# Optimization experiments

Measured on AMD Instinct MI355X. Metric: run time of the kernel, lower is better.

The kernel has to match this reference:

```python
import jax, jax.numpy as jnp
import numpy as np

N_NODES = 50000
N_EDGES = 600000
HIDDEN = 128
NUM_FEAT = 3
NUM_CLASSES = 2
NUM_GRAPHS = 512


def setup_inputs() -> dict:
    key = jax.random.key(0)
    ks = jax.random.split(key, 12)
    x = jax.random.normal(ks[0], (N_NODES, NUM_FEAT), dtype=jnp.float32)
    edge_index = jax.random.randint(ks[1], (2, N_EDGES), 0, N_NODES, dtype=jnp.int64)
    batch = jnp.sort(jax.random.randint(ks[2], (N_NODES,), 0, NUM_GRAPHS, dtype=jnp.int64))

    def glorot(k, fan_in, fan_out):
        s = jnp.sqrt(6.0 / (fan_in + fan_out)).astype(jnp.float32)
        return jax.random.uniform(k, (fan_in, fan_out), jnp.float32, -s, s)

    return {
        "x": x,
        "W1": glorot(ks[3], NUM_FEAT, HIDDEN), "b1": jnp.zeros((HIDDEN,), jnp.float32),
        "W2": glorot(ks[4], HIDDEN, HIDDEN),  "b2": jnp.zeros((HIDDEN,), jnp.float32),
        "W3": glorot(ks[5], HIDDEN, HIDDEN),  "b3": jnp.zeros((HIDDEN,), jnp.float32),
        "W4": glorot(ks[6], HIDDEN, HIDDEN),  "b4": jnp.zeros((HIDDEN,), jnp.float32),
        "linW": glorot(ks[7], HIDDEN, NUM_CLASSES), "linb": jnp.zeros((NUM_CLASSES,), jnp.float32),
        "edge_index": edge_index,
        "batch": batch,
        "num_graphs": NUM_GRAPHS,
    }


def gcn_conv(x, W, b, src, dst, n_nodes):
    # PyG GCNConv: h = x W; out = D^-1/2 (A + I) D^-1/2 h + b
    h = x @ W                                    # [N, out]
    deg = jnp.zeros((n_nodes,), h.dtype).at[dst].add(1.0) + 1.0  # with self-loops
    dinv = jax.lax.rsqrt(deg)                    # [N]
    norm = dinv[src] * dinv[dst]                 # [E]
    msg = h[src] * norm[:, None]                 # gather + scale
    agg = jax.ops.segment_sum(msg, dst, num_segments=n_nodes)  # scatter-add
    agg = agg + h * (dinv * dinv)[:, None]       # self-loop contribution
    return agg + b


def reference(x, W1, b1, W2, b2, W3, b3, W4, b4, linW, linb, edge_index, batch, num_graphs):
    src, dst = edge_index[0], edge_index[1]
    n = x.shape[0]
    h = jax.nn.relu(gcn_conv(x, W1, b1, src, dst, n))
    h = jax.nn.relu(gcn_conv(h, W2, b2, src, dst, n))
    h = jax.nn.relu(gcn_conv(h, W3, b3, src, dst, n))
    h = gcn_conv(h, W4, b4, src, dst, n)
    # global_mean_pool over graphs
    sums = jax.ops.segment_sum(h, batch, num_segments=num_graphs)
    cnts = jax.ops.segment_sum(jnp.ones((n,), h.dtype), batch, num_segments=num_graphs)
    pooled = sums / jnp.maximum(cnts, 1.0)[:, None]
    # dropout is identity in eval mode
    return pooled @ linW + linb
```

## Files before the change

kernel.cpp:

```cpp
#include <hip/hip_runtime.h>
#include <hip/hip_bf16.h>

#define HID 128
#define NGRAPH 512

typedef __attribute__((ext_vector_type(8))) short short8;
typedef __attribute__((ext_vector_type(4))) float f32x4;

__device__ inline unsigned int f2bf(float f) {
    unsigned int u = __float_as_uint(f);
    return (u + 0x7FFFu + ((u >> 16) & 1u)) >> 16;
}
__device__ inline float bflo(unsigned int w) { return __uint_as_float(w << 16); }
__device__ inline float bfhi(unsigned int w) { return __uint_as_float(w & 0xFFFF0000u); }


__global__ void k_zero(int* __restrict__ p, int n) {
    int i = blockIdx.x * blockDim.x + threadIdx.x;
    if (i < n) p[i] = 0;
}

__global__ void k_count(const int* __restrict__ ei, int* __restrict__ deg,
                        int* __restrict__ epos, int E) {
    int e = blockIdx.x * blockDim.x + threadIdx.x;
    if (e < E) epos[e] = atomicAdd(&deg[ei[E + e]], 1);
}

__device__ inline void wcast_body(const float* __restrict__ W,
                                  unsigned short* __restrict__ Wt) {
    int t = threadIdx.x;
#pragma unroll
    for (int i = 0; i < 16; ++i) {
        int flat = i * 1024 + t;
        int n = flat >> 7, k = flat & 127;
        Wt[n * HID + k] = (unsigned short)f2bf(W[k * HID + n]);
    }
}

__global__ void k_bsum(const int* __restrict__ deg, int* __restrict__ bsum, int n,
                       int nblocks, const float* __restrict__ W4,
                       const float* __restrict__ linW, const float* __restrict__ b4,
                       const float* __restrict__ linb, float* __restrict__ W4p,
                       float* __restrict__ b4p, const float* __restrict__ W2,
                       const float* __restrict__ W3, unsigned short* __restrict__ Wt2,
                       unsigned short* __restrict__ Wt3) {
    if ((int)blockIdx.x == nblocks) {
        int idx = threadIdx.x;
        if (idx < 256) {
            int k = idx >> 1, c = idx & 1;
            float a = 0.0f;
            for (int j = 0; j < HID; ++j) a = fmaf(W4[k * HID + j], linW[j * 2 + c], a);
            W4p[idx] = a;
            if (idx < 2) {
                float b = 0.0f;
                for (int j = 0; j < HID; ++j) b = fmaf(b4[j], linW[j * 2 + idx], b);
                b4p[idx] = b + linb[idx];
            }
        }
        return;
    }
    if ((int)blockIdx.x == nblocks + 1) { wcast_body(W2, Wt2); return; }
    if ((int)blockIdx.x == nblocks + 2) { wcast_body(W3, Wt3); return; }
    int i = blockIdx.x * 1024 + threadIdx.x;
    int v = (i < n) ? deg[i] : 0;
#pragma unroll
    for (int off = 32; off; off >>= 1) v += __shfl_down(v, off);
    __shared__ int ws[16];
    int wid = threadIdx.x >> 6, lane = threadIdx.x & 63;
    if (lane == 0) ws[wid] = v;
    __syncthreads();
    if (threadIdx.x == 0) {
        int s = 0;
#pragma unroll
        for (int w = 0; w < 16; ++w) s += ws[w];
        bsum[blockIdx.x] = s;
    }
}

__global__ void k_scan2(const int* __restrict__ deg, const int* __restrict__ bsum,
                        int* __restrict__ row_start, float* __restrict__ dinv,
                        const float* __restrict__ x, float* __restrict__ Xs,
                        int n, int nblocks) {
    __shared__ int s_off, s_tot;
    __shared__ int ws[16];
    if (threadIdx.x < 64) {
        int v = ((int)threadIdx.x < blockIdx.x) ? bsum[threadIdx.x] : 0;
#pragma unroll
        for (int off = 32; off; off >>= 1) v += __shfl_down(v, off);
        if (threadIdx.x == 0) s_off = v;
    } else if (threadIdx.x < 128 && blockIdx.x == 0) {
        int l = threadIdx.x - 64;
        int v = (l < nblocks) ? bsum[l] : 0;
#pragma unroll
        for (int off = 32; off; off >>= 1) v += __shfl_down(v, off);
        if (l == 0) s_tot = v;
    }
    int i = blockIdx.x * 1024 + threadIdx.x;
    int v = (i < n) ? deg[i] : 0;
    if (i < n) {
        float dv = rsqrtf((float)v + 1.0f);
        dinv[i] = dv;
        float4 r;
        r.x = x[i * 3 + 0] * dv;
        r.y = x[i * 3 + 1] * dv;
        r.z = x[i * 3 + 2] * dv;
        r.w = 0.0f;
        *(float4*)&Xs[i * 4] = r;
    }
    int xx = v;
    int lane = threadIdx.x & 63, wid = threadIdx.x >> 6;
#pragma unroll
    for (int off = 1; off < 64; off <<= 1) {
        int t = __shfl_up(xx, off);
        if (lane >= off) xx += t;
    }
    if (lane == 63) ws[wid] = xx;
    __syncthreads();
    int wo = 0;
    for (int w = 0; w < wid; ++w) wo += ws[w];
    int excl = s_off + wo + xx - v;
    if (i < n) row_start[i] = excl;
    if (blockIdx.x == 0 && threadIdx.x == 0) row_start[n] = s_tot;
}

__global__ void k_fill(const int* __restrict__ ei, const int* __restrict__ row_start,
                       const int* __restrict__ epos, int* __restrict__ src_sorted, int E) {
    int e = blockIdx.x * blockDim.x + threadIdx.x;
    if (e < E) {
        int s = ei[e];
        int d = ei[E + e];
        src_sorted[row_start[d] + epos[e]] = s;
    }
}


__global__ __launch_bounds__(256) void k_gather3w(const float* __restrict__ Xs,
                                                  const int* __restrict__ row_start,
                                                  const int* __restrict__ src_sorted,
                                                  const float* __restrict__ dinv,
                                                  float* __restrict__ xa, int n) {
    int t = blockIdx.x * blockDim.x + threadIdx.x;
    int v = t >> 3, sub = t & 7;
    if (v >= n) return;
    float a0 = 0.f, a1 = 0.f, a2 = 0.f;
    int e0 = row_start[v], e1 = row_start[v + 1];
    for (int e = e0 + sub; e < e1; e += 8) {
        int s = src_sorted[e];
        float4 xs = *(const float4*)&Xs[s * 4];
        a0 += xs.x; a1 += xs.y; a2 += xs.z;
    }
#pragma unroll
    for (int off = 4; off; off >>= 1) {
        a0 += __shfl_down(a0, off);
        a1 += __shfl_down(a1, off);
        a2 += __shfl_down(a2, off);
    }
    if (sub == 0) {
        float dv = dinv[v];
        float4 xv = *(const float4*)&Xs[v * 4];
        xa[v * 4 + 0] = (a0 + xv.x) * dv;
        xa[v * 4 + 1] = (a1 + xv.y) * dv;
        xa[v * 4 + 2] = (a2 + xv.z) * dv;
    }
}

__global__ void k_feat(const float* __restrict__ xa, const float* __restrict__ W1,
                       const float* __restrict__ b1, unsigned int* __restrict__ Act16,
                       int n) {
    int idx = blockIdx.x * blockDim.x + threadIdx.x;
    int v = idx >> 6, cp = idx & 63;
    unsigned int w = 0;
    if (v < n) {
        float x0 = xa[v * 4 + 0], x1 = xa[v * 4 + 1], x2 = xa[v * 4 + 2];
        int c0 = cp * 2, c1 = c0 + 1;
        float r0 = fmaf(x0, W1[c0], fmaf(x1, W1[HID + c0], fmaf(x2, W1[2 * HID + c0], b1[c0])));
        float r1 = fmaf(x0, W1[c1], fmaf(x1, W1[HID + c1], fmaf(x2, W1[2 * HID + c1], b1[c1])));
        w = f2bf(fmaxf(r0, 0.f)) | (f2bf(fmaxf(r1, 0.f)) << 16);
    }
    Act16[idx] = w;
}

__global__ __launch_bounds__(256) void k_gemm_mfma(const unsigned short* __restrict__ X,
                                                   const unsigned short* __restrict__ Wtg,
                                                   const float* __restrict__ dinv,
                                                   unsigned short* __restrict__ Hout) {
    __shared__ unsigned short Wt[HID * HID];
    {
        int nrow = threadIdx.x >> 1, s = threadIdx.x & 1;
        int xr = (nrow & 7) << 3;
#pragma unroll
        for (int i = 0; i < 8; ++i) {
            int b16 = s * 64 + i * 8;
            uint4 src = *(const uint4*)&Wtg[nrow * HID + b16];
            *(uint4*)&Wt[nrow * HID + (b16 ^ xr)] = src;
        }
    }
    __syncthreads();

    int w    = threadIdx.x >> 6;
    int lane = threadIdx.x & 63;
    int g    = lane >> 4;
    int mr   = lane & 15;
    size_t row0 = (size_t)blockIdx.x * 64;
    size_t arow = row0 + w * 16 + mr;

    short8 a[4];
#pragma unroll
    for (int ks = 0; ks < 4; ++ks)
        a[ks] = *(const short8*)&X[arow * HID + ks * 32 + g * 8];

    f32x4 acc[8];
#pragma unroll
    for (int nt = 0; nt < 8; ++nt) acc[nt] = (f32x4){0.f, 0.f, 0.f, 0.f};

#pragma unroll
    for (int nt = 0; nt < 8; ++nt) {
        int nrow = nt * 16 + mr;
        int xr = (nrow & 7) << 3;
        short8 b[4];
#pragma unroll
        for (int ks = 0; ks < 4; ++ks)
            b[ks] = *(const short8*)&Wt[nrow * HID + ((ks * 32 + g * 8) ^ xr)];
#pragma unroll
        for (int ks = 0; ks < 4; ++ks)
            acc[nt] = __builtin_amdgcn_mfma_f32_16x16x32_bf16(a[ks], b[ks], acc[nt], 0, 0, 0);
    }

    __syncthreads();
    {
        int rrb = w * 16 + g * 4;
#pragma unroll
        for (int j = 0; j < 4; ++j) {
            int rr = rrb + j;
            float dv = dinv[row0 + rr];
#pragma unroll
            for (int nt = 0; nt < 8; ++nt) {
                int col = nt * 16 + mr;
                int idx = rr * HID + ((col & 7) | ((((col >> 3)) ^ (rr & 7)) << 3));
                Wt[idx] = (unsigned short)f2bf(acc[nt][j] * dv);
            }
        }
    }
    __syncthreads();
    {
        int rr = threadIdx.x >> 2, s = threadIdx.x & 3;
        int xr = (rr & 7) << 3;
#pragma unroll
        for (int i = 0; i < 4; ++i) {
            int b16 = s * 32 + i * 8;
            uint4 v = *(const uint4*)&Wt[rr * HID + (b16 ^ xr)];
            *(uint4*)&Hout[(row0 + rr) * HID + b16] = v;
        }
    }
}

__global__ __launch_bounds__(256) void k_gather(const unsigned short* __restrict__ Hs,
                                                const int* __restrict__ row_start,
                                                const int* __restrict__ src_sorted,
                                                const float* __restrict__ dinv,
                                                const float* __restrict__ bias,
                                                unsigned short* __restrict__ Aout, int n) {
    int wid  = (blockIdx.x * blockDim.x + threadIdx.x) >> 6;
    int lane = threadIdx.x & 63;
    int half = lane >> 5, hl = lane & 31;
    int v0 = wid * 2;
    if (v0 >= n) return;
    int v  = v0 + half;
    bool real = (v < n);
    int vc = real ? v : v0;
    int e0 = row_start[vc];
    int e1 = row_start[vc + 1];
    int deg = e1 - e0;
    int myidx = (hl < deg) ? src_sorted[e0 + hl] : vc;
    float4 acc = make_float4(0.f, 0.f, 0.f, 0.f);
    int dcap = (deg < 32) ? deg : 32;
    for (int base = 0; base < dcap; base += 16) {
        uint2 h[16];
        float m[16];
#pragma unroll
        for (int j = 0; j < 16; ++j) {
            int ej = base + j;
            int sj = __shfl(myidx, (half << 5) | ej);
            m[j] = (ej < deg) ? 1.0f : 0.0f;
            h[j] = *(const uint2*)&Hs[(size_t)sj * HID + hl * 4];
        }
#pragma unroll
        for (int j = 0; j < 16; ++j) {
            acc.x = fmaf(bflo(h[j].x), m[j], acc.x);
            acc.y = fmaf(bfhi(h[j].x), m[j], acc.y);
            acc.z = fmaf(bflo(h[j].y), m[j], acc.z);
            acc.w = fmaf(bfhi(h[j].y), m[j], acc.w);
        }
    }
    for (int e = e0 + 32; e < e1; ++e) {
        int sj = src_sorted[e];
        uint2 h = *(const uint2*)&Hs[(size_t)sj * HID + hl * 4];
        acc.x += bflo(h.x); acc.y += bfhi(h.x);
        acc.z += bflo(h.y); acc.w += bfhi(h.y);
    }
    float dv = dinv[vc];
    uint2 sv = *(const uint2*)&Hs[(size_t)vc * HID + hl * 4];
    float4 bb = *(const float4*)&bias[hl * 4];
    float ox = fmaxf(fmaf(acc.x + bflo(sv.x), dv, bb.x), 0.0f);
    float oy = fmaxf(fmaf(acc.y + bfhi(sv.x), dv, bb.y), 0.0f);
    float oz = fmaxf(fmaf(acc.z + bflo(sv.y), dv, bb.z), 0.0f);
    float ow = fmaxf(fmaf(acc.w + bfhi(sv.y), dv, bb.w), 0.0f);
    if (real) {
        uint2 o2;
        o2.x = f2bf(ox) | (f2bf(oy) << 16);
        o2.y = f2bf(oz) | (f2bf(ow) << 16);
        *(uint2*)&Aout[(size_t)v * HID + hl * 4] = o2;
    }
}

__global__ __launch_bounds__(256) void k_gather_proj(const unsigned short* __restrict__ Hs,
                                                     const int* __restrict__ row_start,
                                                     const int* __restrict__ src_sorted,
                                                     const float* __restrict__ dinv,
                                                     const float* __restrict__ bias,
                                                     const float* __restrict__ W4p,
                                                     float* __restrict__ P3s, int n) {
    int wid  = (blockIdx.x * blockDim.x + threadIdx.x) >> 6;
    int lane = threadIdx.x & 63;
    int half = lane >> 5, hl = lane & 31;
    int v0 = wid * 2;
    if (v0 >= n) return;
    int v  = v0 + half;
    bool real = (v < n);
    int vc = real ? v : v0;
    int e0 = row_start[vc];
    int e1 = row_start[vc + 1];
    int deg = e1 - e0;
    int myidx = (hl < deg) ? src_sorted[e0 + hl] : vc;
    float4 acc = make_float4(0.f, 0.f, 0.f, 0.f);
    int dcap = (deg < 32) ? deg : 32;
    for (int base = 0; base < dcap; base += 16) {
        uint2 h[16];
        float m[16];
#pragma unroll
        for (int j = 0; j < 16; ++j) {
            int ej = base + j;
            int sj = __shfl(myidx, (half << 5) | ej);
            m[j] = (ej < deg) ? 1.0f : 0.0f;
            h[j] = *(const uint2*)&Hs[(size_t)sj * HID + hl * 4];
        }
#pragma unroll
        for (int j = 0; j < 16; ++j) {
            acc.x = fmaf(bflo(h[j].x), m[j], acc.x);
            acc.y = fmaf(bfhi(h[j].x), m[j], acc.y);
            acc.z = fmaf(bflo(h[j].y), m[j], acc.z);
            acc.w = fmaf(bfhi(h[j].y), m[j], acc.w);
        }
    }
    for (int e = e0 + 32; e < e1; ++e) {
        int sj = src_sorted[e];
        uint2 h = *(const uint2*)&Hs[(size_t)sj * HID + hl * 4];
        acc.x += bflo(h.x); acc.y += bfhi(h.x);
        acc.z += bflo(h.y); acc.w += bfhi(h.y);
    }
    float dv = dinv[vc];
    uint2 sv = *(const uint2*)&Hs[(size_t)vc * HID + hl * 4];
    float4 bb = *(const float4*)&bias[hl * 4];
    float ox = fmaxf(fmaf(acc.x + bflo(sv.x), dv, bb.x), 0.0f);
    float oy = fmaxf(fmaf(acc.y + bfhi(sv.x), dv, bb.y), 0.0f);
    float oz = fmaxf(fmaf(acc.z + bflo(sv.y), dv, bb.z), 0.0f);
    float ow = fmaxf(fmaf(acc.w + bfhi(sv.y), dv, bb.w), 0.0f);
    float4 wA = *(const float4*)&W4p[hl * 8 + 0];
    float4 wB = *(const float4*)&W4p[hl * 8 + 4];
    float p0 = ox * wA.x + oy * wA.z + oz * wB.x + ow * wB.z;
    float p1 = ox * wA.y + oy * wA.w + oz * wB.y + ow * wB.w;
#pragma unroll
    for (int off = 16; off; off >>= 1) {
        p0 += __shfl_down(p0, off);
        p1 += __shfl_down(p1, off);
    }
    if (hl == 0 && real) *(float2*)&P3s[v * 2] = make_float2(p0 * dv, p1 * dv);
}

__global__ __launch_bounds__(256) void k_gather2(const float* __restrict__ P3s,
                                                 const int* __restrict__ row_start,
                                                 const int* __restrict__ src_sorted,
                                                 const float* __restrict__ dinv,
                                                 float* __restrict__ A2, int n) {
    int t = blockIdx.x * blockDim.x + threadIdx.x;
    int v = t >> 3, sub = t & 7;
    if (v >= n) return;
    float ax = 0.f, ay = 0.f;
    int e0 = row_start[v], e1 = row_start[v + 1];
    for (int e = e0 + sub; e < e1; e += 8) {
        int s = src_sorted[e];
        float2 ps = *(const float2*)&P3s[s * 2];
        ax += ps.x;
        ay += ps.y;
    }
#pragma unroll
    for (int off = 4; off; off >>= 1) {
        ax += __shfl_down(ax, off);
        ay += __shfl_down(ay, off);
    }
    if (sub == 0) {
        float dv = dinv[v];
        float2 pv = *(const float2*)&P3s[v * 2];
        *(float2*)&A2[v * 2] = make_float2((ax + pv.x) * dv, (ay + pv.y) * dv);
    }
}

__global__ void k_poolg(const float* __restrict__ A2, const int* __restrict__ batch,
                        const float* __restrict__ b4p, float* __restrict__ out, int n) {
    int g = blockIdx.x;
    int lane = threadIdx.x;
    int lo = 0, hi = n;
    while (lo < hi) { int m = (lo + hi) >> 1; if (batch[m] < g) lo = m + 1; else hi = m; }
    int start = lo;
    hi = n;
    while (lo < hi) { int m = (lo + hi) >> 1; if (batch[m] < g + 1) lo = m + 1; else hi = m; }
    int end = lo;
    float sx = 0.f, sy = 0.f;
    for (int i = start + lane; i < end; i += 64) {
        float2 a = *(const float2*)&A2[i * 2];
        sx += a.x;
        sy += a.y;
    }
#pragma unroll
    for (int off = 32; off; off >>= 1) {
        sx += __shfl_down(sx, off);
        sy += __shfl_down(sy, off);
    }
    if (lane == 0) {
        float inv = 1.0f / fmaxf((float)(end - start), 1.0f);
        out[g * 2 + 0] = sx * inv + b4p[0];
        out[g * 2 + 1] = sy * inv + b4p[1];
    }
}


extern "C" void kernel_launch(void* const* d_in, const int* in_sizes, int n_in,
                              void* d_out, int out_size, void* d_ws, size_t ws_size,
                              hipStream_t stream) {
    const float* x    = (const float*)d_in[0];
    const float* W1   = (const float*)d_in[1];
    const float* b1   = (const float*)d_in[2];
    const float* W2   = (const float*)d_in[3];
    const float* b2   = (const float*)d_in[4];
    const float* W3   = (const float*)d_in[5];
    const float* b3   = (const float*)d_in[6];
    const float* W4   = (const float*)d_in[7];
    const float* b4   = (const float*)d_in[8];
    const float* linW = (const float*)d_in[9];
    const float* linb = (const float*)d_in[10];
    const int*   ei   = (const int*)d_in[11];
    const int*   batch= (const int*)d_in[12];
    float* out        = (float*)d_out;

    const int N = in_sizes[0] / 3;
    const int E = in_sizes[11] / 2;
    const int NPAD = ((N + 127) / 128) * 128;
    const int NB1024 = (N + 1023) / 1024;

    float* ws = (float*)d_ws;
    float* dinv       = ws;
    int*   deg_i      = (int*)(ws + 50176);
    int*   row_start  = (int*)(ws + 100352);
    int*   epos       = (int*)(ws + 150784);
    int*   bsum       = (int*)(ws + 750848);
    float* W4p        = ws + 750912;
    float* b4p        = ws + 751168;
    int*   src_sorted = (int*)(ws + 751232);
    float* Xa         = ws + 1351296;
    float* A2         = Xa;
    float* P3s        = ws + 1552000;
    unsigned short* Hbuf16 = (unsigned short*)(ws + 1652352);
    float* Xs         = ws + 1652352;
    unsigned short* Act16 = (unsigned short*)(ws + 1652352 + (size_t)NPAD * 64);
    unsigned short* Wt2g  = (unsigned short*)(ws + 1652352 + 2 * (size_t)NPAD * 64);
    unsigned short* Wt3g  = Wt2g + HID * HID;

    const int B = 256;

    k_zero<<<(N + B - 1) / B, B, 0, stream>>>(deg_i, N);
    k_count<<<(E + B - 1) / B, B, 0, stream>>>(ei, deg_i, epos, E);
    k_bsum<<<NB1024 + 3, 1024, 0, stream>>>(deg_i, bsum, N, NB1024, W4, linW, b4, linb,
                                            W4p, b4p, W2, W3, Wt2g, Wt3g);
    k_scan2<<<NB1024, 1024, 0, stream>>>(deg_i, bsum, row_start, dinv, x, Xs, N, NB1024);
    k_fill<<<(E + B - 1) / B, B, 0, stream>>>(ei, row_start, epos, src_sorted, E);

    const int gatherBlocks = (N + 7) / 8;
    const int g8Blocks     = (N * 8 + B - 1) / B;
    const int gemmBlocks   = NPAD / 64;

    k_gather3w<<<g8Blocks, B, 0, stream>>>(Xs, row_start, src_sorted, dinv, Xa, N);
    k_feat<<<(NPAD * 64) / B, B, 0, stream>>>(Xa, W1, b1, (unsigned int*)Act16, N);
    k_gemm_mfma<<<gemmBlocks, B, 0, stream>>>(Act16, Wt2g, dinv, Hbuf16);
    k_gather<<<gatherBlocks, B, 0, stream>>>(Hbuf16, row_start, src_sorted, dinv, b2, Act16, N);
    k_gemm_mfma<<<gemmBlocks, B, 0, stream>>>(Act16, Wt3g, dinv, Hbuf16);
    k_gather_proj<<<gatherBlocks, B, 0, stream>>>(Hbuf16, row_start, src_sorted, dinv, b3, W4p, P3s, N);
    k_gather2<<<g8Blocks, B, 0, stream>>>(P3s, row_start, src_sorted, dinv, A2, N);
    k_poolg<<<NGRAPH, 64, 0, stream>>>(A2, batch, b4p, out, N);
}
```

Measured before the change: 169.4 us.

## Fuse setup, layer-1 and tail kernels to cut launch count

Measured after the change: 169.8 us. About the same (+0.3%).

```diff
diff --git a/kernel.cpp b/kernel.cpp
--- a/kernel.cpp
+++ b/kernel.cpp
@@ -14,17 +14,6 @@
 __device__ inline float bflo(unsigned int w) { return __uint_as_float(w << 16); }
 __device__ inline float bfhi(unsigned int w) { return __uint_as_float(w & 0xFFFF0000u); }
 
-
-__global__ void k_zero(int* __restrict__ p, int n) {
-    int i = blockIdx.x * blockDim.x + threadIdx.x;
-    if (i < n) p[i] = 0;
-}
-
-__global__ void k_count(const int* __restrict__ ei, int* __restrict__ deg,
-                        int* __restrict__ epos, int E) {
-    int e = blockIdx.x * blockDim.x + threadIdx.x;
-    if (e < E) epos[e] = atomicAdd(&deg[ei[E + e]], 1);
-}
 
 __device__ inline void wcast_body(const float* __restrict__ W,
                                   unsigned short* __restrict__ Wt) {
@@ -37,14 +26,13 @@
     }
 }
 
-__global__ void k_bsum(const int* __restrict__ deg, int* __restrict__ bsum, int n,
-                       int nblocks, const float* __restrict__ W4,
-                       const float* __restrict__ linW, const float* __restrict__ b4,
-                       const float* __restrict__ linb, float* __restrict__ W4p,
-                       float* __restrict__ b4p, const float* __restrict__ W2,
-                       const float* __restrict__ W3, unsigned short* __restrict__ Wt2,
-                       unsigned short* __restrict__ Wt3) {
-    if ((int)blockIdx.x == nblocks) {
+__global__ void k_setup1(int* __restrict__ deg, int n, int nzb,
+                         const float* __restrict__ W4, const float* __restrict__ linW,
+                         const float* __restrict__ b4, const float* __restrict__ linb,
+                         float* __restrict__ W4p, float* __restrict__ b4p,
+                         const float* __restrict__ W2, const float* __restrict__ W3,
+                         unsigned short* __restrict__ Wt2, unsigned short* __restrict__ Wt3) {
+    if ((int)blockIdx.x == nzb) {
         int idx = threadIdx.x;
         if (idx < 256) {
             int k = idx >> 1, c = idx & 1;
@@ -59,41 +47,40 @@
         }
         return;
     }
-    if ((int)blockIdx.x == nblocks + 1) { wcast_body(W2, Wt2); return; }
-    if ((int)blockIdx.x == nblocks + 2) { wcast_body(W3, Wt3); return; }
+    if ((int)blockIdx.x == nzb + 1) { wcast_body(W2, Wt2); return; }
+    if ((int)blockIdx.x == nzb + 2) { wcast_body(W3, Wt3); return; }
     int i = blockIdx.x * 1024 + threadIdx.x;
-    int v = (i < n) ? deg[i] : 0;
-#pragma unroll
-    for (int off = 32; off; off >>= 1) v += __shfl_down(v, off);
+    if (i < n) deg[i] = 0;
+}
+
+__global__ void k_count(const int* __restrict__ ei, int* __restrict__ deg,
+                        int* __restrict__ epos, int E) {
+    int e = blockIdx.x * blockDim.x + threadIdx.x;
+    if (e < E) epos[e] = atomicAdd(&deg[ei[E + e]], 1);
+}
+
+__global__ void k_scan2b(const int* __restrict__ deg, int* __restrict__ row_start,
+                         float* __restrict__ dinv, const float* __restrict__ x,
+                         float* __restrict__ Xs, int n, int nblocks) {
+    __shared__ int rs[16];
     __shared__ int ws[16];
-    int wid = threadIdx.x >> 6, lane = threadIdx.x & 63;
-    if (lane == 0) ws[wid] = v;
-    __syncthreads();
-    if (threadIdx.x == 0) {
-        int s = 0;
-#pragma unroll
-        for (int w = 0; w < 16; ++w) s += ws[w];
-        bsum[blockIdx.x] = s;
-    }
-}
-
-__global__ void k_scan2(const int* __restrict__ deg, const int* __restrict__ bsum,
-                        int* __restrict__ row_start, float* __restrict__ dinv,
-                        const float* __restrict__ x, float* __restrict__ Xs,
-                        int n, int nblocks) {
-    __shared__ int s_off, s_tot;
-    __shared__ int ws[16];
-    if (threadIdx.x < 64) {
-        int v = ((int)threadIdx.x < blockIdx.x) ? bsum[threadIdx.x] : 0;
-#pragma unroll
-        for (int off = 32; off; off >>= 1) v += __shfl_down(v, off);
-        if (threadIdx.x == 0) s_off = v;
-    } else if (threadIdx.x < 128 && blockIdx.x == 0) {
-        int l = threadIdx.x - 64;
-        int v = (l < nblocks) ? bsum[l] : 0;
-#pragma unroll
-        for (int off = 32; off; off >>= 1) v += __shfl_down(v, off);
-        if (l == 0) s_tot = v;
+    __shared__ int s_off_sh;
+    int lane = threadIdx.x & 63, wid = threadIdx.x >> 6;
+    {
+        int before = blockIdx.x * 1024;
+        int p = 0;
+        for (int i = threadIdx.x; i < before; i += 1024) p += deg[i];
+#pragma unroll
+        for (int off = 32; off; off >>= 1) p += __shfl_down(p, off);
+        if (lane == 0) rs[wid] = p;
+        __syncthreads();
+        if (threadIdx.x == 0) {
+            int s = 0;
+#pragma unroll
+            for (int w = 0; w < 16; ++w) s += rs[w];
+            s_off_sh = s;
+        }
+        __syncthreads();
     }
     int i = blockIdx.x * 1024 + threadIdx.x;
     int v = (i < n) ? deg[i] : 0;
@@ -108,7 +95,6 @@
         *(float4*)&Xs[i * 4] = r;
     }
     int xx = v;
-    int lane = threadIdx.x & 63, wid = threadIdx.x >> 6;
 #pragma unroll
     for (int off = 1; off < 64; off <<= 1) {
         int t = __shfl_up(xx, off);
@@ -118,9 +104,14 @@
     __syncthreads();
     int wo = 0;
     for (int w = 0; w < wid; ++w) wo += ws[w];
-    int excl = s_off + wo + xx - v;
+    int excl = s_off_sh + wo + xx - v;
     if (i < n) row_start[i] = excl;
-    if (blockIdx.x == 0 && threadIdx.x == 0) row_start[n] = s_tot;
+    if ((int)blockIdx.x == nblocks - 1 && threadIdx.x == 0) {
+        int ct = 0;
+#pragma unroll
+        for (int w = 0; w < 16; ++w) ct += ws[w];
+        row_start[n] = s_off_sh + ct;
+    }
 }
 
 __global__ void k_fill(const int* __restrict__ ei, const int* __restrict__ row_start,
@@ -133,21 +124,25 @@
     }
 }
 
-
-__global__ __launch_bounds__(256) void k_gather3w(const float* __restrict__ Xs,
-                                                  const int* __restrict__ row_start,
-                                                  const int* __restrict__ src_sorted,
-                                                  const float* __restrict__ dinv,
-                                                  float* __restrict__ xa, int n) {
-    int t = blockIdx.x * blockDim.x + threadIdx.x;
-    int v = t >> 3, sub = t & 7;
-    if (v >= n) return;
+__global__ __launch_bounds__(256) void k_l1(const float* __restrict__ Xs,
+                                            const int* __restrict__ row_start,
+                                            const int* __restrict__ src_sorted,
+                                            const float* __restrict__ dinv,
+                                            const float* __restrict__ W1,
+                                            const float* __restrict__ b1,
+                                            unsigned int* __restrict__ Act16, int n) {
+    __shared__ float xs[32][4];
+    int v0 = blockIdx.x * 32;
+    int vl0 = threadIdx.x >> 3, sub = threadIdx.x & 7;
+    int v = v0 + vl0;
     float a0 = 0.f, a1 = 0.f, a2 = 0.f;
-    int e0 = row_start[v], e1 = row_start[v + 1];
-    for (int e = e0 + sub; e < e1; e += 8) {
-        int s = src_sorted[e];
-        float4 xs = *(const float4*)&Xs[s * 4];
-        a0 += xs.x; a1 += xs.y; a2 += xs.z;
+    if (v < n) {
+        int e0 = row_start[v], e1 = row_start[v + 1];
+        for (int e = e0 + sub; e < e1; e += 8) {
+            int s = src_sorted[e];
+            float4 xv = *(const float4*)&Xs[s * 4];
+            a0 += xv.x; a1 += xv.y; a2 += xv.z;
+        }
     }
 #pragma unroll
     for (int off = 4; off; off >>= 1) {
@@ -155,29 +150,29 @@
         a1 += __shfl_down(a1, off);
         a2 += __shfl_down(a2, off);
     }
-    if (sub == 0) {
+    if (sub == 0 && v < n) {
         float dv = dinv[v];
         float4 xv = *(const float4*)&Xs[v * 4];
-        xa[v * 4 + 0] = (a0 + xv.x) * dv;
-        xa[v * 4 + 1] = (a1 + xv.y) * dv;
-        xa[v * 4 + 2] = (a2 + xv.z) * dv;
-    }
-}
-
-__global__ void k_feat(const float* __restrict__ xa, const float* __restrict__ W1,
-                       const float* __restrict__ b1, unsigned int* __restrict__ Act16,
-                       int n) {
-    int idx = blockIdx.x * blockDim.x + threadIdx.x;
-    int v = idx >> 6, cp = idx & 63;
-    unsigned int w = 0;
-    if (v < n) {
-        float x0 = xa[v * 4 + 0], x1 = xa[v * 4 + 1], x2 = xa[v * 4 + 2];
-        int c0 = cp * 2, c1 = c0 + 1;
-        float r0 = fmaf(x0, W1[c0], fmaf(x1, W1[HID + c0], fmaf(x2, W1[2 * HID + c0], b1[c0])));
-        float r1 = fmaf(x0, W1[c1], fmaf(x1, W1[HID + c1], fmaf(x2, W1[2 * HID + c1], b1[c1])));
-        w = f2bf(fmaxf(r0, 0.f)) | (f2bf(fmaxf(r1, 0.f)) << 16);
-    }
-    Act16[idx] = w;
+        xs[vl0][0] = (a0 + xv.x) * dv;
+        xs[vl0][1] = (a1 + xv.y) * dv;
+        xs[vl0][2] = (a2 + xv.z) * dv;
+    }
+    __syncthreads();
+    unsigned int base = (unsigned int)v0 * 64;
+#pragma unroll
+    for (int i = 0; i < 8; ++i) {
+        int flat = i * 256 + threadIdx.x;
+        int vl = flat >> 6, cp = flat & 63;
+        unsigned int w = 0;
+        if (v0 + vl < n) {
+            float x0 = xs[vl][0], x1 = xs[vl][1], x2 = xs[vl][2];
+            int c0 = cp * 2, c1 = c0 + 1;
+            float r0 = fmaf(x0, W1[c0], fmaf(x1, W1[HID + c0], fmaf(x2, W1[2 * HID + c0], b1[c0])));
+            float r1 = fmaf(x0, W1[c1], fmaf(x1, W1[HID + c1], fmaf(x2, W1[2 * HID + c1], b1[c1])));
+            w = f2bf(fmaxf(r0, 0.f)) | (f2bf(fmaxf(r1, 0.f)) << 16);
+        }
+        Act16[base + flat] = w;
+    }
 }
 
 __global__ __launch_bounds__(256) void k_gemm_mfma(const unsigned short* __restrict__ X,
@@ -377,59 +372,60 @@
     if (hl == 0 && real) *(float2*)&P3s[v * 2] = make_float2(p0 * dv, p1 * dv);
 }
 
-__global__ __launch_bounds__(256) void k_gather2(const float* __restrict__ P3s,
-                                                 const int* __restrict__ row_start,
-                                                 const int* __restrict__ src_sorted,
-                                                 const float* __restrict__ dinv,
-                                                 float* __restrict__ A2, int n) {
-    int t = blockIdx.x * blockDim.x + threadIdx.x;
-    int v = t >> 3, sub = t & 7;
-    if (v >= n) return;
-    float ax = 0.f, ay = 0.f;
-    int e0 = row_start[v], e1 = row_start[v + 1];
-    for (int e = e0 + sub; e < e1; e += 8) {
-        int s = src_sorted[e];
-        float2 ps = *(const float2*)&P3s[s * 2];
-        ax += ps.x;
-        ay += ps.y;
-    }
-#pragma unroll
-    for (int off = 4; off; off >>= 1) {
-        ax += __shfl_down(ax, off);
-        ay += __shfl_down(ay, off);
-    }
-    if (sub == 0) {
-        float dv = dinv[v];
-        float2 pv = *(const float2*)&P3s[v * 2];
-        *(float2*)&A2[v * 2] = make_float2((ax + pv.x) * dv, (ay + pv.y) * dv);
-    }
-}
-
-__global__ void k_poolg(const float* __restrict__ A2, const int* __restrict__ batch,
-                        const float* __restrict__ b4p, float* __restrict__ out, int n) {
+__global__ __launch_bounds__(256) void k_tail(const float* __restrict__ P3s,
+                                              const int* __restrict__ row_start,
+                                              const int* __restrict__ src_sorted,
+                                              const float* __restrict__ dinv,
+                                              const int* __restrict__ batch,
+                                              const float* __restrict__ b4p,
+                                              float* __restrict__ out, int n) {
     int g = blockIdx.x;
-    int lane = threadIdx.x;
     int lo = 0, hi = n;
     while (lo < hi) { int m = (lo + hi) >> 1; if (batch[m] < g) lo = m + 1; else hi = m; }
     int start = lo;
     hi = n;
     while (lo < hi) { int m = (lo + hi) >> 1; if (batch[m] < g + 1) lo = m + 1; else hi = m; }
     int end = lo;
-    float sx = 0.f, sy = 0.f;
-    for (int i = start + lane; i < end; i += 64) {
-        float2 a = *(const float2*)&A2[i * 2];
-        sx += a.x;
-        sy += a.y;
-    }
-#pragma unroll
-    for (int off = 32; off; off >>= 1) {
-        sx += __shfl_down(sx, off);
-        sy += __shfl_down(sy, off);
-    }
-    if (lane == 0) {
-        float inv = 1.0f / fmaxf((float)(end - start), 1.0f);
-        out[g * 2 + 0] = sx * inv + b4p[0];
-        out[g * 2 + 1] = sy * inv + b4p[1];
+
+    int grp = threadIdx.x >> 3, sub = threadIdx.x & 7;
+    float gx = 0.f, gy = 0.f;
+    for (int v = start + grp; v < end; v += 32) {
+        float ax = 0.f, ay = 0.f;
+        int e0 = row_start[v], e1 = row_start[v + 1];
+        for (int e = e0 + sub; e < e1; e += 8) {
+            int s = src_sorted[e];
+            float2 ps = *(const float2*)&P3s[s * 2];
+            ax += ps.x;
+            ay += ps.y;
+        }
+#pragma unroll
+        for (int off = 4; off; off >>= 1) {
+            ax += __shfl_down(ax, off);
+            ay += __shfl_down(ay, off);
+        }
+        if (sub == 0) {
+            float dv = dinv[v];
+            float2 pv = *(const float2*)&P3s[v * 2];
+            gx += (ax + pv.x) * dv;
+            gy += (ay + pv.y) * dv;
+        }
+    }
+    __shared__ float red[64];
+    if (sub == 0) { red[grp] = gx; red[grp + 32] = gy; }
+    __syncthreads();
+    if (threadIdx.x < 64) {
+        float sx = (threadIdx.x < 32) ? red[threadIdx.x] : 0.f;
+        float sy = (threadIdx.x < 32) ? red[threadIdx.x + 32] : 0.f;
+#pragma unroll
+        for (int off = 16; off; off >>= 1) {
+            sx += __shfl_down(sx, off);
+            sy += __shfl_down(sy, off);
+        }
+        if (threadIdx.x == 0) {
+            float inv = 1.0f / fmaxf((float)(end - start), 1.0f);
+            out[g * 2 + 0] = sx * inv + b4p[0];
+            out[g * 2 + 1] = sy * inv + b4p[1];
+        }
     }
 }
 
@@ -466,34 +462,30 @@
     float* W4p        = ws + 750912;
     float* b4p        = ws + 751168;
     int*   src_sorted = (int*)(ws + 751232);
-    float* Xa         = ws + 1351296;
-    float* A2         = Xa;
     float* P3s        = ws + 1552000;
     unsigned short* Hbuf16 = (unsigned short*)(ws + 1652352);
     float* Xs         = ws + 1652352;
     unsigned short* Act16 = (unsigned short*)(ws + 1652352 + (size_t)NPAD * 64);
     unsigned short* Wt2g  = (unsigned short*)(ws + 1652352 + 2 * (size_t)NPAD * 64);
     unsigned short* Wt3g  = Wt2g + HID * HID;
+    (void)bsum;
 
     const int B = 256;
 
-    k_zero<<<(N + B - 1) / B, B, 0, stream>>>(deg_i, N);
+    k_setup1<<<NB1024 + 3, 1024, 0, stream>>>(deg_i, N, NB1024, W4, linW, b4, linb,
+                                              W4p, b4p, W2, W3, Wt2g, Wt3g);
     k_count<<<(E + B - 1) / B, B, 0, stream>>>(ei, deg_i, epos, E);
-    k_bsum<<<NB1024 + 3, 1024, 0, stream>>>(deg_i, bsum, N, NB1024, W4, linW, b4, linb,
-                                            W4p, b4p, W2, W3, Wt2g, Wt3g);
-    k_scan2<<<NB1024, 1024, 0, stream>>>(deg_i, bsum, row_start, dinv, x, Xs, N, NB1024);
+    k_scan2b<<<NB1024, 1024, 0, stream>>>(deg_i, row_start, dinv, x, Xs, N, NB1024);
     k_fill<<<(E + B - 1) / B, B, 0, stream>>>(ei, row_start, epos, src_sorted, E);
 
     const int gatherBlocks = (N + 7) / 8;
-    const int g8Blocks     = (N * 8 + B - 1) / B;
     const int gemmBlocks   = NPAD / 64;
 
-    k_gather3w<<<g8Blocks, B, 0, stream>>>(Xs, row_start, src_sorted, dinv, Xa, N);
-    k_feat<<<(NPAD * 64) / B, B, 0, stream>>>(Xa, W1, b1, (unsigned int*)Act16, N);
+    k_l1<<<NPAD / 32, B, 0, stream>>>(Xs, row_start, src_sorted, dinv, W1, b1,
+                                      (unsigned int*)Act16, N);
     k_gemm_mfma<<<gemmBlocks, B, 0, stream>>>(Act16, Wt2g, dinv, Hbuf16);
     k_gather<<<gatherBlocks, B, 0, stream>>>(Hbuf16, row_start, src_sorted, dinv, b2, Act16, N);
     k_gemm_mfma<<<gemmBlocks, B, 0, stream>>>(Act16, Wt3g, dinv, Hbuf16);
     k_gather_proj<<<gatherBlocks, B, 0, stream>>>(Hbuf16, row_start, src_sorted, dinv, b3, W4p, P3s, N);
-    k_gather2<<<g8Blocks, B, 0, stream>>>(P3s, row_start, src_sorted, dinv, A2, N);
-    k_poolg<<<NGRAPH, 64, 0, stream>>>(A2, batch, b4p, out, N);
-}
+    k_tail<<<NGRAPH, B, 0, stream>>>(P3s, row_start, src_sorted, dinv, batch, b4p, out, N);
+}
```
